# Performance work log

Measured on AMD Instinct MI355X. Metric: run time of the kernel, lower is better.

The kernel has to match this reference:

```python
import jax, jax.numpy as jnp
import numpy as np

GEMMA2_TANH_SCALE = 50.0
N_HEADS = 16
HEAD_DIM = 128
NEG_INF = -1e9


def setup_inputs() -> dict:
    key = jax.random.key(0)
    ks = jax.random.split(key, 5)
    B, S, D = 2, 2048, 2048
    H, HD = N_HEADS, HEAD_DIM
    x = jax.random.normal(ks[0], (B, S, D), jnp.float32)
    w_scale = 1.0 / np.sqrt(D)
    wq = jax.random.normal(ks[1], (H * HD, D), jnp.float32) * w_scale
    wk = jax.random.normal(ks[2], (H * HD, D), jnp.float32) * w_scale
    wv = jax.random.normal(ks[3], (H * HD, D), jnp.float32) * w_scale
    wo = jax.random.normal(ks[4], (D, H * HD), jnp.float32) * w_scale
    # RoPE frequencies: standard llama theta=10000, [S, HD/2, (cos,sin)]
    inv_freq = 1.0 / (10000.0 ** (np.arange(0, HD, 2, dtype=np.float32) / HD))
    ang = np.outer(np.arange(S, dtype=np.float32), inv_freq)  # [S, HD/2]
    freqs_cis = jnp.asarray(np.stack([np.cos(ang), np.sin(ang)], axis=-1), jnp.float32)
    # causal additive mask [1,1,S,S]
    causal = np.tril(np.ones((S, S), dtype=bool))
    mask = jnp.asarray(np.where(causal, 0.0, NEG_INF).astype(np.float32))[None, None]
    return {"x": x, "freqs_cis": freqs_cis, "mask": mask,
            "wq": wq, "wk": wk, "wv": wv, "wo": wo}


def _apply_rope(t, freqs_cis):
    # t: [B,S,H,HD]; treat adjacent pairs as complex, multiply by e^{i*ang}
    B, S, H, HD = t.shape
    tr = t.reshape(B, S, H, HD // 2, 2)
    a, b = tr[..., 0], tr[..., 1]
    cos = freqs_cis[None, :, None, :, 0]
    sin = freqs_cis[None, :, None, :, 1]
    out = jnp.stack([a * cos - b * sin, a * sin + b * cos], axis=-1)
    return out.reshape(B, S, H, HD)


def reference(x, freqs_cis, mask, wq, wk, wv, wo):
    B, S, D = x.shape
    H, HD = N_HEADS, HEAD_DIM
    xq = (x @ wq.T).reshape(B, S, H, HD)
    xk = (x @ wk.T).reshape(B, S, H, HD)
    xv = (x @ wv.T).reshape(B, S, H, HD)
    q = _apply_rope(xq, freqs_cis).transpose(0, 2, 1, 3)  # [B,H,S,HD]
    k = _apply_rope(xk, freqs_cis).transpose(0, 2, 1, 3)
    v = xv.transpose(0, 2, 1, 3)
    scores = jnp.einsum('bhqd,bhkd->bhqk', q, k) / np.sqrt(HD).astype(np.float32)
    # gemma2 tanh softcap
    scores = jnp.tanh(scores / GEMMA2_TANH_SCALE) * GEMMA2_TANH_SCALE
    scores = scores + mask
    probs = jax.nn.softmax(scores.astype(jnp.float32), axis=-1).astype(q.dtype)
    out = jnp.einsum('bhqk,bhkd->bhqd', probs, v)
    out = out.transpose(0, 2, 1, 3).reshape(B, S, H * HD)
    return out @ wo.T
```

## Files before the change

kernel.cpp:

```cpp
#include <hip/hip_runtime.h>
#include <hip/hip_bf16.h>
#include <stdint.h>

#define DEVI __device__ __forceinline__

typedef __attribute__((ext_vector_type(8))) short bf16x8;
typedef __attribute__((ext_vector_type(4))) short bf16x4;
typedef __attribute__((ext_vector_type(4))) float f32x4;

static constexpr int S_  = 2048;
static constexpr int H_  = 16;
static constexpr int HD_ = 128;

DEVI short f2bf(float f){
  uint32_t u = __builtin_bit_cast(uint32_t, f);
  u += 0x7fffu + ((u >> 16) & 1u);
  return (short)(u >> 16);
}
DEVI float bf2f(short s){
  uint32_t u = ((uint32_t)(uint16_t)s) << 16;
  return __builtin_bit_cast(float, u);
}

DEVI void gll16(const short* g, const short* lds_base){
  __builtin_amdgcn_global_load_lds(
      (const __attribute__((address_space(1))) void*)g,
      (__attribute__((address_space(3))) void*)lds_base,
      16, 0, 0);
}

__global__ __launch_bounds__(256)
void cvt6_kernel(const float* __restrict__ x,  const float* __restrict__ wq,
                 const float* __restrict__ wk, const float* __restrict__ wv,
                 const float* __restrict__ wo,
                 short* __restrict__ XB, short* __restrict__ WQKV, short* __restrict__ WO)
{
  const float* src; short* dst;
  switch (blockIdx.y){
    case 0:  src = x;           dst = XB;             break;
    case 1:  src = x + 4194304; dst = XB + 4194304;   break;
    case 2:  src = wq;          dst = WQKV;           break;
    case 3:  src = wk;          dst = WQKV + 4194304; break;
    case 4:  src = wv;          dst = WQKV + 8388608; break;
    default: src = wo;          dst = WO;             break;
  }
  int i = blockIdx.x * 256 + threadIdx.x;
  float4 v = ((const float4*)src)[i];
  bf16x4 o;
  o[0] = f2bf(v.x); o[1] = f2bf(v.y); o[2] = f2bf(v.z); o[3] = f2bf(v.w);
  ((bf16x4*)dst)[i] = o;
}

template<int EPI>
__global__ __launch_bounds__(256)
void gemm_bt(const short* __restrict__ A, const short* __restrict__ Bw,
             float* __restrict__ Cout, short* __restrict__ Qo,
             short* __restrict__ Ko, short* __restrict__ Vo,
             int M, int N, int K)
{
  __shared__ short As[128*32];
  __shared__ short Bs[128*32];
  int tiles_m = M >> 7;
  int bm = (int)blockIdx.x % tiles_m;
  int bn = (int)blockIdx.x / tiles_m;
  int tid = threadIdx.x;
  int w = tid >> 6, l = tid & 63;
  int l15 = l & 15, lg = l >> 4;
  int wr = w >> 1, wc = w & 1;

  f32x4 acc[4][4];
#pragma unroll
  for (int i = 0; i < 4; ++i)
#pragma unroll
    for (int j = 0; j < 4; ++j) acc[i][j] = 0;

  for (int k0 = 0; k0 < K; k0 += 32){
#pragma unroll
    for (int j = 0; j < 2; ++j){
      int c = j*256 + w*64 + l;
      int row = c >> 2, kc = c & 3;
      gll16(A  + ((size_t)(bm*128 + row))*K + k0 + kc*8, As + (j*256 + w*64)*8);
      gll16(Bw + ((size_t)(bn*128 + row))*K + k0 + kc*8, Bs + (j*256 + w*64)*8);
    }
    __syncthreads();
    bf16x8 af[4], bfv[4];
#pragma unroll
    for (int i = 0; i < 4; ++i){
      af[i]  = *(const bf16x8*)(As + (wr*64 + i*16 + l15)*32 + lg*8);
      bfv[i] = *(const bf16x8*)(Bs + (wc*64 + i*16 + l15)*32 + lg*8);
    }
#pragma unroll
    for (int i = 0; i < 4; ++i)
#pragma unroll
      for (int j = 0; j < 4; ++j)
        acc[i][j] = __builtin_amdgcn_mfma_f32_16x16x32_bf16(af[i], bfv[j], acc[i][j], 0, 0, 0);
    __syncthreads();
  }

#pragma unroll
  for (int i = 0; i < 4; ++i){
#pragma unroll
    for (int j = 0; j < 4; ++j){
      int m0 = bm*128 + wr*64 + i*16 + lg*4;
      int n  = bn*128 + wc*64 + j*16 + l15;
      if (EPI == 0){
#pragma unroll
        for (int r = 0; r < 4; ++r)
          Cout[(size_t)(m0 + r)*N + n] = acc[i][j][r];
      } else {
        int sect = n >> 11;
        int nn = n & 2047;
        int h = nn >> 7, d = nn & 127;
        if (sect == 2){
          int b = m0 >> 11, s = m0 & 2047;
          bf16x4 pv;
#pragma unroll
          for (int r = 0; r < 4; ++r) pv[r] = f2bf(acc[i][j][r]);
          *(bf16x4*)(Vo + (((size_t)(b*H_ + h))*HD_ + d)*S_ + s) = pv;
        } else {
          short* dst = (sect == 0) ? Qo : Ko;
#pragma unroll
          for (int r = 0; r < 4; ++r){
            int m = m0 + r; int b = m >> 11, s = m & 2047;
            dst[(((size_t)(b*H_ + h))*S_ + s)*HD_ + d] = f2bf(acc[i][j][r]);
          }
        }
      }
    }
  }
}

__global__ __launch_bounds__(256)
void rope_kernel(short* __restrict__ q, short* __restrict__ k,
                 const float* __restrict__ fr){
  int idx = blockIdx.x * 256 + threadIdx.x;
  short* p = (blockIdx.y == 0) ? q : k;
  int t = idx & 15, row = idx >> 4;
  int s = row & (S_ - 1);
  short* ptr = p + (size_t)row*HD_ + t*8;
  bf16x8 v = *(bf16x8*)ptr;
  const float* f = fr + ((size_t)s*64 + t*4)*2;
  float4 f0 = *(const float4*)f;
  float4 f1 = *(const float4*)(f + 4);
  bf16x8 o;
  float a, b;
  a = bf2f(v[0]); b = bf2f(v[1]); o[0] = f2bf(a*f0.x - b*f0.y); o[1] = f2bf(a*f0.y + b*f0.x);
  a = bf2f(v[2]); b = bf2f(v[3]); o[2] = f2bf(a*f0.z - b*f0.w); o[3] = f2bf(a*f0.w + b*f0.z);
  a = bf2f(v[4]); b = bf2f(v[5]); o[4] = f2bf(a*f1.x - b*f1.y); o[5] = f2bf(a*f1.y + b*f1.x);
  a = bf2f(v[6]); b = bf2f(v[7]); o[6] = f2bf(a*f1.z - b*f1.w); o[7] = f2bf(a*f1.w + b*f1.z);
  *(bf16x8*)ptr = o;
}

__global__ __launch_bounds__(256)
void attn_kernel(const short* __restrict__ Q, const short* __restrict__ Kg,
                 const short* __restrict__ Vt, short* __restrict__ Ob)
{
  __shared__ short Ks[64*136];
  __shared__ short Vs[128*72];
  __shared__ short Ps[4][16*72];
  int bx = blockIdx.x, bh = blockIdx.y;
  int tid = threadIdx.x;
  int w = tid >> 6, l = tid & 63, l15 = l & 15, lg = l >> 4;
  int b = bh >> 4, h = bh & 15;
  const float C1 = 0.0051007025f;

  for (int pass = 0; pass < 2; ++pass){
    int qt = pass ? (31 - bx) : bx;
    int q0 = qt*64 + w*16;

    bf16x8 qf[4];
    {
      const short* qp = Q + ((size_t)bh*S_ + q0 + l15)*HD_ + lg*8;
#pragma unroll
      for (int kc = 0; kc < 4; ++kc) qf[kc] = *(const bf16x8*)(qp + kc*32);
    }
    f32x4 o[8];
#pragma unroll
    for (int dt = 0; dt < 8; ++dt) o[dt] = 0;
    float lp[4];
#pragma unroll
    for (int r = 0; r < 4; ++r) lp[r] = 0.f;

    for (int kt = 0; kt <= qt; ++kt){
      int kv0 = kt*64;
      __syncthreads();
#pragma unroll
      for (int j = 0; j < 4; ++j){
        int c = tid + j*256; int row = c >> 4, k8 = c & 15;
        *(bf16x8*)(Ks + row*136 + k8*8) =
          *(const bf16x8*)(Kg + ((size_t)bh*S_ + kv0 + row)*HD_ + k8*8);
      }
#pragma unroll
      for (int j = 0; j < 4; ++j){
        int c = tid + j*256; int d = c >> 3, k8 = c & 7;
        *(bf16x8*)(Vs + d*72 + k8*8) =
          *(const bf16x8*)(Vt + ((size_t)bh*HD_ + d)*S_ + kv0 + k8*8);
      }
      __syncthreads();

      f32x4 sa[4];
#pragma unroll
      for (int tj = 0; tj < 4; ++tj) sa[tj] = 0;
#pragma unroll
      for (int tj = 0; tj < 4; ++tj)
#pragma unroll
        for (int kc = 0; kc < 4; ++kc){
          bf16x8 kf = *(const bf16x8*)(Ks + (tj*16 + l15)*136 + kc*32 + lg*8);
          sa[tj] = __builtin_amdgcn_mfma_f32_16x16x32_bf16(qf[kc], kf, sa[tj], 0, 0, 0);
        }

#pragma unroll
      for (int tj = 0; tj < 4; ++tj)
#pragma unroll
        for (int r = 0; r < 4; ++r){
          float e1 = exp2f(sa[tj][r] * C1) + 1.0f;
          float rc = __fdividef(144.269504f, e1);
          float p  = exp2f(72.134752f - rc);
          if (kt == qt){
            int kcol = kv0 + tj*16 + l15;
            int qrow = q0 + lg*4 + r;
            if (kcol > qrow) p = 0.f;
          }
          lp[r] += p;
          sa[tj][r] = p;
        }

      short* ps = &Ps[w][0];
#pragma unroll
      for (int tj = 0; tj < 4; ++tj)
#pragma unroll
        for (int r = 0; r < 4; ++r){
          int row = lg*4 + r;
          int col = tj*16 + l15;
          ps[row*72 + (col ^ ((row & 8) << 1))] = f2bf(sa[tj][r]);
        }
      bf16x8 pa0 = *(const bf16x8*)(ps + l15*72 + ((lg*8)      ^ ((l15 & 8) << 1)));
      bf16x8 pa1 = *(const bf16x8*)(ps + l15*72 + ((32 + lg*8) ^ ((l15 & 8) << 1)));

#pragma unroll
      for (int dt = 0; dt < 8; ++dt){
        bf16x8 v0 = *(const bf16x8*)(Vs + (dt*16 + l15)*72 + lg*8);
        bf16x8 v1 = *(const bf16x8*)(Vs + (dt*16 + l15)*72 + 32 + lg*8);
        o[dt] = __builtin_amdgcn_mfma_f32_16x16x32_bf16(pa0, v0, o[dt], 0, 0, 0);
        o[dt] = __builtin_amdgcn_mfma_f32_16x16x32_bf16(pa1, v1, o[dt], 0, 0, 0);
      }
    }

    float inv[4];
#pragma unroll
    for (int r = 0; r < 4; ++r){
      float ts = lp[r];
#pragma unroll
      for (int off = 1; off < 16; off <<= 1) ts += __shfl_xor(ts, off, 64);
      inv[r] = __fdividef(1.0f, ts);
    }
#pragma unroll
    for (int dt = 0; dt < 8; ++dt)
#pragma unroll
      for (int r = 0; r < 4; ++r){
        int qrow = q0 + lg*4 + r;
        Ob[((size_t)(b*S_ + qrow))*(H_*HD_) + h*HD_ + dt*16 + l15] = f2bf(o[dt][r] * inv[r]);
      }
  }
}

extern "C" void kernel_launch(void* const* d_in, const int* in_sizes, int n_in,
                              void* d_out, int out_size, void* d_ws, size_t ws_size,
                              hipStream_t stream)
{
  const float* x  = (const float*)d_in[0];
  const float* fr = (const float*)d_in[1];
  const float* wq = (const float*)d_in[3];
  const float* wk = (const float*)d_in[4];
  const float* wv = (const float*)d_in[5];
  const float* wo = (const float*)d_in[6];
  float* out = (float*)d_out;

  char* ws = (char*)d_ws;
  short* XB   = (short*)(ws + 0);
  short* WQKV = (short*)(ws + 16777216);
  short* WO   = (short*)(ws + 41943040);
  short* QB   = (short*)(ws + 50331648);
  short* KB   = (short*)(ws + 67108864);
  short* VT   = (short*)(ws + 83886080);
  short* AB   = (short*)(ws + 0);

  cvt6_kernel<<<dim3(4096, 6), 256, 0, stream>>>(x, wq, wk, wv, wo, XB, WQKV, WO);
  gemm_bt<1><<<dim3(32*48), 256, 0, stream>>>(XB, WQKV, nullptr, QB, KB, VT, 4096, 6144, 2048);
  rope_kernel<<<dim3(4096, 2), 256, 0, stream>>>(QB, KB, fr);
  attn_kernel<<<dim3(16, 32), 256, 0, stream>>>(QB, KB, VT, AB);
  gemm_bt<0><<<dim3(32*16), 256, 0, stream>>>(AB, WO, out, nullptr, nullptr, nullptr, 4096, 2048, 2048);
}
```

Measured before the change: 499.5 us.

## Load K and V fragments directly from global memory into registers, dropping LDS staging

The attention kernel no longer stages K and V tiles in shared memory behind block-wide barriers. Each wave now loads its MFMA operand fragments for K and transposed V straight from global memory into registers, with the V loads issued before the softmax so they can overlap it. This removes the LDS round trip and two __syncthreads per KV tile. In exchange, each of the four waves reads the same K/V data from global memory or L2, which quadruples that traffic, and the 32 extra vector registers per lane may lower occupancy.

```diff
diff --git a/kernel.cpp b/kernel.cpp
--- a/kernel.cpp
+++ b/kernel.cpp
@@ -155,8 +155,6 @@
 void attn_kernel(const short* __restrict__ Q, const short* __restrict__ Kg,
                  const short* __restrict__ Vt, short* __restrict__ Ob)
 {
-  __shared__ short Ks[64*136];
-  __shared__ short Vs[128*72];
   __shared__ short Ps[4][16*72];
   int bx = blockIdx.x, bh = blockIdx.y;
   int tid = threadIdx.x;
@@ -164,6 +162,9 @@
   int b = bh >> 4, h = bh & 15;
   const float C1 = 0.0051007025f;
 
+  const short* kbh = Kg + (size_t)bh*S_*HD_;
+  const short* vbh = Vt + (size_t)bh*HD_*S_;
+
   for (int pass = 0; pass < 2; ++pass){
     int qt = pass ? (31 - bx) : bx;
     int q0 = qt*64 + w*16;
@@ -183,20 +184,14 @@
 
     for (int kt = 0; kt <= qt; ++kt){
       int kv0 = kt*64;
-      __syncthreads();
-#pragma unroll
-      for (int j = 0; j < 4; ++j){
-        int c = tid + j*256; int row = c >> 4, k8 = c & 15;
-        *(bf16x8*)(Ks + row*136 + k8*8) =
-          *(const bf16x8*)(Kg + ((size_t)bh*S_ + kv0 + row)*HD_ + k8*8);
-      }
-#pragma unroll
-      for (int j = 0; j < 4; ++j){
-        int c = tid + j*256; int d = c >> 3, k8 = c & 7;
-        *(bf16x8*)(Vs + d*72 + k8*8) =
-          *(const bf16x8*)(Vt + ((size_t)bh*HD_ + d)*S_ + kv0 + k8*8);
-      }
-      __syncthreads();
+
+      bf16x8 kf[16];
+      const short* kb = kbh + (size_t)(kv0 + l15)*HD_ + lg*8;
+#pragma unroll
+      for (int tj = 0; tj < 4; ++tj)
+#pragma unroll
+        for (int kc = 0; kc < 4; ++kc)
+          kf[tj*4+kc] = *(const bf16x8*)(kb + tj*16*HD_ + kc*32);
 
       f32x4 sa[4];
 #pragma unroll
@@ -204,10 +199,16 @@
 #pragma unroll
       for (int tj = 0; tj < 4; ++tj)
 #pragma unroll
-        for (int kc = 0; kc < 4; ++kc){
-          bf16x8 kf = *(const bf16x8*)(Ks + (tj*16 + l15)*136 + kc*32 + lg*8);
-          sa[tj] = __builtin_amdgcn_mfma_f32_16x16x32_bf16(qf[kc], kf, sa[tj], 0, 0, 0);
-        }
+        for (int kc = 0; kc < 4; ++kc)
+          sa[tj] = __builtin_amdgcn_mfma_f32_16x16x32_bf16(qf[kc], kf[tj*4+kc], sa[tj], 0, 0, 0);
+
+      bf16x8 vf[16];
+      const short* vb = vbh + (size_t)l15*S_ + kv0 + lg*8;
+#pragma unroll
+      for (int dt = 0; dt < 8; ++dt)
+#pragma unroll
+        for (int hf = 0; hf < 2; ++hf)
+          vf[dt*2+hf] = *(const bf16x8*)(vb + (size_t)dt*16*S_ + hf*32);
 
 #pragma unroll
       for (int tj = 0; tj < 4; ++tj)
@@ -239,10 +240,8 @@
 
 #pragma unroll
       for (int dt = 0; dt < 8; ++dt){
-        bf16x8 v0 = *(const bf16x8*)(Vs + (dt*16 + l15)*72 + lg*8);
-        bf16x8 v1 = *(const bf16x8*)(Vs + (dt*16 + l15)*72 + 32 + lg*8);
-        o[dt] = __builtin_amdgcn_mfma_f32_16x16x32_bf16(pa0, v0, o[dt], 0, 0, 0);
-        o[dt] = __builtin_amdgcn_mfma_f32_16x16x32_bf16(pa1, v1, o[dt], 0, 0, 0);
+        o[dt] = __builtin_amdgcn_mfma_f32_16x16x32_bf16(pa0, vf[dt*2+0], o[dt], 0, 0, 0);
+        o[dt] = __builtin_amdgcn_mfma_f32_16x16x32_bf16(pa1, vf[dt*2+1], o[dt], 0, 0, 0);
       }
     }
 
```

After: 597.9 us. +19.7%, slower.
